# Performance work log

Hardware: AMD Instinct MI355X
Metric: run time of the kernel (lower is better)

The kernel has to match this reference:

```python
import jax, jax.numpy as jnp
import numpy as np

LN_EPS = 1e-5
NEG_INF = -1e30


def setup_inputs() -> dict:
    key = jax.random.key(0)
    k_adj, k_feat, k_mask, k_w = jax.random.split(key, 4)
    B, N, H, R, L = 8, 400, 768, 46, 2
    adj = jax.random.uniform(k_adj, (B, N, N, R), dtype=jnp.float32)
    feature = jax.random.normal(k_feat, (B, N, H), dtype=jnp.float32)
    dmask = (jax.random.uniform(k_mask, (B, 1, N)) > 0.1).astype(jnp.float32)
    # per-layer, per-relation Linear(H, H, bias=False) weights, applied as x @ W
    W = jax.random.normal(k_w, (L, R, H, H), dtype=jnp.float32) / np.sqrt(H)
    return {"adj": adj, "feature": feature, "dmask": dmask, "W": W}


def reference(adj, feature, dmask, W):
    # adj: [B,N,N,R] -> [B,R,N,N]; dmask: [B,1,N] masks key/column axis
    B, N, _, R = adj.shape
    a = jnp.transpose(adj, (0, 3, 1, 2))           # [B,R,N,N]
    m = dmask[:, None, :, :]                        # [B,1,1,N]
    logits = a * m + (1.0 - m) * NEG_INF
    att = jax.nn.softmax(logits, axis=-1)           # [B,R,N,N] (layer-invariant)

    x = feature
    num_layers = W.shape[0]
    for layer in range(num_layers):
        # grouped per-relation linear: h[b,r,n,k] = feature[b,n,h] @ W[layer,r,h,k]
        h = jnp.einsum('bnh,rhk->brnk', x, W[layer])
        h = jax.nn.relu(jnp.einsum('brnm,brmk->brnk', att, h))
        addition = h.sum(axis=1)                    # sum over relations -> [B,N,H]
        z = jax.nn.relu(addition) / R
        # LayerNorm without affine params
        mu = jnp.mean(z, axis=-1, keepdims=True)
        var = jnp.var(z, axis=-1, keepdims=True)
        x = (z - mu) / jnp.sqrt(var + LN_EPS)
        # dropout is identity in eval mode
    return x
```

## Files before the change

kernel.cpp:

```cpp
#include <hip/hip_runtime.h>
#include <stdint.h>

#define BS 8
#define NN 400
#define HH 768
#define RR 46
#define MPAD 416
#define MFLAT2 3328
#define LDW2 3328
#define PADM 402

typedef _Float16 half8 __attribute__((ext_vector_type(8)));
typedef _Float16 half4v __attribute__((ext_vector_type(4)));
typedef float floatx4 __attribute__((ext_vector_type(4)));

__device__ __forceinline__ void async16(const void* g, void* l) {
  __builtin_amdgcn_global_load_lds((const __attribute__((address_space(1))) uint32_t*)g,
                                   (__attribute__((address_space(3))) uint32_t*)l, 16, 0, 0);
}

__device__ __forceinline__ int xcd_work(int flat, int nwg) {
  int q = nwg >> 3, rem = nwg & 7;
  int xcd = flat & 7, slot = flat >> 3;
  return (xcd < rem ? xcd * (q + 1) : rem * (q + 1) + (xcd - rem) * q) + slot;
}

__device__ __forceinline__ void vm_wait(int ahead) {
  if (ahead >= 2) asm volatile("s_waitcnt vmcnt(8)" ::: "memory");
  else if (ahead == 1) asm volatile("s_waitcnt vmcnt(4)" ::: "memory");
  else asm volatile("s_waitcnt vmcnt(0)" ::: "memory");
}
__device__ __forceinline__ void vm_wait2(int ahead) {
  if (ahead >= 2) asm volatile("s_waitcnt vmcnt(4)" ::: "memory");
  else if (ahead == 1) asm volatile("s_waitcnt vmcnt(2)" ::: "memory");
  else asm volatile("s_waitcnt vmcnt(0)" ::: "memory");
}
#define BAR_TOP() { __builtin_amdgcn_s_barrier(); __builtin_amdgcn_sched_barrier(0); }
#define BAR_BOT() { asm volatile("s_waitcnt lgkmcnt(0)" ::: "memory"); \
                    __builtin_amdgcn_s_barrier(); __builtin_amdgcn_sched_barrier(0); }
#define BAR_ONE() { asm volatile("s_barrier" ::: "memory"); __builtin_amdgcn_sched_barrier(0); }

__device__ __forceinline__ void stage_tile(const _Float16* __restrict__ g, int ld, int rowbase,
                                           int maxrow, int kbase, _Float16* lds, int t) {
  int w = t >> 6, lane = t & 63;
#pragma unroll
  for (int j = 0; j < 2; ++j) {
    int chunk = w * 2 + j;
    int eo = chunk * 512 + lane * 8;
    int row = eo >> 5;
    int col = eo & 31;
    int grow = rowbase + row;
    grow = grow > maxrow ? maxrow : grow;
    async16(g + (size_t)grow * ld + kbase + col, lds + chunk * 512);
  }
}

__device__ __forceinline__ void mma_tiles(const _Float16* As, const _Float16* Bs, int lane,
                                          int wr, int wc, floatx4 acc[4][4]) {
  int arow = wr + (lane & 15);
  int brow = wc + (lane & 15);
  int kcol = (lane >> 4) * 8;
  half8 a[4], b[4];
#pragma unroll
  for (int i = 0; i < 4; ++i) a[i] = *(const half8*)&As[(arow + i * 16) * 32 + kcol];
#pragma unroll
  for (int i = 0; i < 4; ++i) b[i] = *(const half8*)&Bs[(brow + i * 16) * 32 + kcol];
#pragma unroll
  for (int i = 0; i < 4; ++i)
#pragma unroll
    for (int j = 0; j < 4; ++j)
      acc[i][j] = __builtin_amdgcn_mfma_f32_16x16x32_f16(a[i], b[j], acc[i][j], 0, 0, 0);
}

__device__ __forceinline__ void mma8(const _Float16* As, const _Float16* Bs, int lane,
                                     int wr, int wc, floatx4 acc[4][2]) {
  int arow = wr + (lane & 15);
  int brow = wc + (lane & 15);
  int kcol = (lane >> 4) * 8;
  half8 a[4], b[2];
#pragma unroll
  for (int i = 0; i < 4; ++i) a[i] = *(const half8*)&As[(arow + i * 16) * 32 + kcol];
#pragma unroll
  for (int j = 0; j < 2; ++j) b[j] = *(const half8*)&Bs[(brow + j * 16) * 32 + kcol];
#pragma unroll
  for (int i = 0; i < 4; ++i)
#pragma unroll
    for (int j = 0; j < 2; ++j)
      acc[i][j] = __builtin_amdgcn_mfma_f32_16x16x32_f16(a[i], b[j], acc[i][j], 0, 0, 0);
}

__global__ __launch_bounds__(256) void conv_w(const float* __restrict__ W, _Float16* __restrict__ Wt) {
  __shared__ float tl[32][33];
  int t = threadIdx.x;
  int lr = blockIdx.y;
  int tr = blockIdx.x / 24, tc = blockIdx.x % 24;
  const float* src = W + (size_t)lr * HH * HH;
  _Float16* dst = Wt + (size_t)lr * HH * HH;
  int rl = t >> 5, cl = t & 31;
#pragma unroll
  for (int j = 0; j < 4; ++j)
    tl[rl + 8 * j][cl] = src[(size_t)(tr * 32 + rl + 8 * j) * HH + tc * 32 + cl];
  __syncthreads();
#pragma unroll
  for (int j = 0; j < 4; ++j)
    dst[(size_t)(tc * 32 + rl + 8 * j) * HH + tr * 32 + cl] = (_Float16)tl[cl][rl + 8 * j];
}

__global__ void conv_x(const float* __restrict__ f, _Float16* __restrict__ x16) {
  int i4 = blockIdx.x * 256 + threadIdx.x;
  int row = i4 / 192;
  int c4 = i4 - row * 192;
  int b = row / 416;
  int m = row - b * 416;
  half4v h = {};
  if (m < NN) {
    float4 v = *(const float4*)(f + ((size_t)(b * NN + m) * HH) + c4 * 4);
    h[0] = (_Float16)v.x; h[1] = (_Float16)v.y; h[2] = (_Float16)v.z; h[3] = (_Float16)v.w;
  }
  *(half4v*)&x16[(size_t)row * HH + c4 * 4] = h;
}

__global__ __launch_bounds__(512) void att_softmax(const float* __restrict__ adj,
                                                   const float* __restrict__ dmask,
                                                   _Float16* __restrict__ att) {
  __shared__ _Float16 sE[RR * PADM];
  __shared__ float sM[NN];
  int t = threadIdx.x;
  int n = blockIdx.x, b = blockIdx.y;
  const float* arow = adj + ((size_t)b * NN + n) * NN * RR;
  for (int i = t; i < NN; i += 512) sM[i] = dmask[b * NN + i];
  __syncthreads();
  for (int e0 = t * 4; e0 < NN * RR; e0 += 2048) {
    float4 v = *(const float4*)(arow + e0);
    float vv[4] = {v.x, v.y, v.z, v.w};
#pragma unroll
    for (int j = 0; j < 4; ++j) {
      int e = e0 + j;
      int m = e / RR;
      int r = e - m * RR;
      float val = sM[m] > 0.5f ? __expf(vv[j]) : 0.0f;
      sE[r * PADM + m] = (_Float16)val;
    }
  }
  __syncthreads();
  int lane = t & 63, wid = t >> 6;
  for (int r = wid; r < RR; r += 8) {
    const _Float16* row = &sE[r * PADM];
    float s = 0.f;
    for (int m = lane; m < NN; m += 64) s += (float)row[m];
#pragma unroll
    for (int o = 32; o; o >>= 1) s += __shfl_xor(s, o);
    float inv = 1.0f / s;
    _Float16* orow = att + (((size_t)b * RR + r) * NN + n) * MPAD;
    for (int m2 = lane * 2; m2 < MPAD; m2 += 128) {
      _Float16 lo = (_Float16)0.f, hi = (_Float16)0.f;
      if (m2 < NN) lo = (_Float16)((float)row[m2] * inv);
      if (m2 + 1 < NN) hi = (_Float16)((float)row[m2 + 1] * inv);
      union { _Float16 h[2]; uint32_t u; } pk;
      pk.h[0] = lo; pk.h[1] = hi;
      *(uint32_t*)&orow[m2] = pk.u;
    }
  }
}

__global__ __launch_bounds__(256) void gemm_xw(const _Float16* __restrict__ x16,
                                               const _Float16* __restrict__ Wt,
                                               _Float16* __restrict__ h1T, int layer, int r0, int rbase) {
  __shared__ __align__(16) char smraw[49152];
  int t = threadIdx.x;
  int work = xcd_work(blockIdx.x, gridDim.x);
  int r_i = work / 156;
  int rem = work - r_i * 156;
  int r = r0 + r_i;
  int mtile = rem / 6, ntile = rem % 6;
  const _Float16* A = x16;
  const _Float16* Bp = Wt + ((size_t)layer * RR + r) * HH * HH;
  int lane = t & 63, w = t >> 6;
  int wr = (w >> 1) * 64, wc = (w & 1) * 64;
  floatx4 acc[4][4] = {};
  stage_tile(A, HH, mtile * 128, MFLAT2 - 1, 0, (_Float16*)smraw, t);
  stage_tile(Bp, HH, ntile * 128, HH - 1, 0, (_Float16*)(smraw + 8192), t);
  stage_tile(A, HH, mtile * 128, MFLAT2 - 1, 32, (_Float16*)(smraw + 16384), t);
  stage_tile(Bp, HH, ntile * 128, HH - 1, 32, (_Float16*)(smraw + 24576), t);
  int cur = 0, stb = 2;
  for (int ks = 0; ks < 24; ++ks) {
    if (ks + 2 < 24) {
      char* nb = smraw + stb * 16384;
      stage_tile(A, HH, mtile * 128, MFLAT2 - 1, (ks + 2) * 32, (_Float16*)nb, t);
      stage_tile(Bp, HH, ntile * 128, HH - 1, (ks + 2) * 32, (_Float16*)(nb + 8192), t);
      stb = stb == 2 ? 0 : stb + 1;
    }
    vm_wait(ks + 2 < 24 ? 2 : (ks + 1 < 24 ? 1 : 0));
    BAR_TOP();
    char* cb = smraw + cur * 16384;
    mma_tiles((const _Float16*)cb, (const _Float16*)(cb + 8192), lane, wr, wc, acc);
    BAR_BOT();
    cur = cur == 2 ? 0 : cur + 1;
  }
  _Float16* outl = (_Float16*)smraw;
#pragma unroll
  for (int i = 0; i < 4; ++i) {
#pragma unroll
    for (int j = 0; j < 4; ++j) {
      int rl = wr + i * 16 + (lane >> 4) * 4;
      int cl = wc + j * 16 + (lane & 15);
      half4v v = {(_Float16)acc[i][j][0], (_Float16)acc[i][j][1],
                  (_Float16)acc[i][j][2], (_Float16)acc[i][j][3]};
      *(half4v*)&outl[cl * 136 + rl] = v;
    }
  }
  __syncthreads();
  _Float16* outp = h1T + (size_t)(r - rbase) * HH * LDW2;
#pragma unroll
  for (int pass = 0; pass < 8; ++pass) {
    int c = pass * 16 + (t >> 4);
    int ml = (t & 15) * 8;
    int gm = mtile * 128 + ml;
    int gn = ntile * 128 + c;
    half8 v = *(const half8*)&outl[c * 136 + ml];
    *(half8*)&outp[(size_t)gn * LDW2 + gm] = v;
  }
}

__global__ __launch_bounds__(512, 4) void gemm_att(const _Float16* __restrict__ att,
                                                   const _Float16* __restrict__ h1T,
                                                   float* __restrict__ partials, size_t psz,
                                                   int rs, int rcount, int rbase, int accflag,
                                                   int ngroups) {
  __shared__ __align__(16) char smraw[65536];
  int t = threadIdx.x;
  int work = xcd_work(blockIdx.x, gridDim.x);
  int ntile = work % 6;
  int tmp = work / 6;
  int mtile = tmp & 3; tmp >>= 2;
  int g = tmp % ngroups;
  int b = tmp / ngroups;
  int rbeg = rs + (g * rcount) / ngroups;
  int rend = rs + ((g + 1) * rcount) / ngroups;
  int nr = rend - rbeg;
  int total = nr * 13;
  float* part = partials + (size_t)g * psz;
  int lane = t & 63, w = t >> 6;
  int wr = (w >> 2) * 64, wc = (w & 3) * 32;
  floatx4 acc[4][2] = {}, sum[4][2] = {};

  int srow = w * 16 + (lane >> 2), scol = (lane & 3) * 8;
  int ga = mtile * 128 + srow; ga = ga > NN - 1 ? NN - 1 : ga;
  int gb = ntile * 128 + srow;
  const _Float16* pa = att + ((size_t)b * RR + rbeg) * NN * MPAD + (size_t)ga * MPAD + scol;
  const _Float16* pb = h1T + (size_t)(rbeg - rbase) * HH * LDW2 + (size_t)gb * LDW2 + b * MPAD + scol;
  int nsk = 0;
  auto issue = [&](int buf) {
    char* lb = smraw + (buf << 14) + w * 1024;
    async16(pa, lb);
    async16(pb, lb + 8192);
    if (++nsk == 13) { nsk = 0; pa += (size_t)NN * MPAD - 384; pb += (size_t)HH * LDW2 - 384; }
    else { pa += 32; pb += 32; }
  };

  issue(0); issue(1); issue(2);
  vm_wait2(2);
  BAR_ONE();
  int cks = 0;
  for (int s = 0; s < total; ++s) {
    if (s + 3 < total) issue((s + 3) & 3);
    char* cb = smraw + ((s & 3) << 14);
    __builtin_amdgcn_s_setprio(1);
    mma8((const _Float16*)cb, (const _Float16*)(cb + 8192), lane, wr, wc, acc);
    __builtin_amdgcn_s_setprio(0);
    if (cks == 12) {
#pragma unroll
      for (int i = 0; i < 4; ++i)
#pragma unroll
        for (int j = 0; j < 2; ++j) {
#pragma unroll
          for (int q2 = 0; q2 < 4; ++q2) sum[i][j][q2] += fmaxf(acc[i][j][q2], 0.0f);
          acc[i][j] = (floatx4){0.f, 0.f, 0.f, 0.f};
        }
      cks = 0;
    } else ++cks;
    if (s + 1 < total) {
      int ahead = total - s - 2;
      vm_wait2(ahead > 2 ? 2 : ahead);
      BAR_ONE();
    }
  }
#pragma unroll
  for (int i = 0; i < 4; ++i) {
    int rl = wr + i * 16 + (lane >> 4) * 4;
    int grow = mtile * 128 + rl;
#pragma unroll
    for (int j = 0; j < 2; ++j) {
      int gcol = ntile * 128 + wc + j * 16 + (lane & 15);
#pragma unroll
      for (int q2 = 0; q2 < 4; ++q2) {
        if (grow + q2 < NN) {
          size_t idx = ((size_t)b * NN + grow + q2) * HH + gcol;
          float v = sum[i][j][q2];
          if (accflag) v += part[idx];
          part[idx] = v;
        }
      }
    }
  }
}

__global__ __launch_bounds__(256) void lnorm(const float* __restrict__ partials, size_t psz, int np,
                                             _Float16* __restrict__ x16, float* __restrict__ out) {
  int row = blockIdx.x;
  int t = threadIdx.x;
  int b = row / NN;
  int xrow = row + b * 16;
  float v[3];
  float s = 0.f, s2 = 0.f;
#pragma unroll
  for (int j = 0; j < 3; ++j) {
    float a = 0.f;
    for (int gidx = 0; gidx < np; ++gidx) a += partials[(size_t)gidx * psz + (size_t)row * HH + t + j * 256];
    v[j] = fmaxf(a, 0.f) * (1.0f / RR);
    s += v[j];
    s2 += v[j] * v[j];
  }
#pragma unroll
  for (int o = 32; o; o >>= 1) {
    s += __shfl_xor(s, o);
    s2 += __shfl_xor(s2, o);
  }
  __shared__ float rs_[4], rs2_[4];
  int lane = t & 63, wid = t >> 6;
  if (!lane) { rs_[wid] = s; rs2_[wid] = s2; }
  __syncthreads();
  s = rs_[0] + rs_[1] + rs_[2] + rs_[3];
  s2 = rs2_[0] + rs2_[1] + rs2_[2] + rs2_[3];
  float mu = s * (1.0f / HH);
  float var = s2 * (1.0f / HH) - mu * mu;
  float rstd = rsqrtf(var + 1e-5f);
#pragma unroll
  for (int j = 0; j < 3; ++j) {
    float o = (v[j] - mu) * rstd;
    out[(size_t)row * HH + t + j * 256] = o;
    x16[(size_t)xrow * HH + t + j * 256] = (_Float16)o;
  }
}

extern "C" void kernel_launch(void* const* d_in, const int* in_sizes, int n_in,
                              void* d_out, int out_size, void* d_ws, size_t ws_size,
                              hipStream_t stream) {
  const float* adj = (const float*)d_in[0];
  const float* feature = (const float*)d_in[1];
  const float* dmask = (const float*)d_in[2];
  const float* W = (const float*)d_in[3];
  float* out = (float*)d_out;

  uintptr_t base = (uintptr_t)d_ws;
  uintptr_t p = base;
  auto alloc = [&](size_t bytes) -> void* {
    uintptr_t q = (p + 255) & ~(uintptr_t)255;
    p = q + bytes;
    return (void*)q;
  };
  _Float16* att = (_Float16*)alloc((size_t)BS * RR * NN * MPAD * 2);
  _Float16* Wt = (_Float16*)alloc((size_t)2 * RR * HH * HH * 2);
  _Float16* x16 = (_Float16*)alloc((size_t)MFLAT2 * HH * 2);
  size_t psz = (size_t)(BS * NN) * HH;
  size_t pszB = psz * 4;
  size_t used = p - base;
  size_t rem = ws_size > used ? ws_size - used : 0;
  size_t perR = (size_t)HH * LDW2 * 2;
  size_t h1full = (size_t)RR * perR;

  conv_w<<<dim3(576, 2 * RR), 256, 0, stream>>>(W, Wt);
  conv_x<<<MFLAT2 * HH / 4 / 256, 256, 0, stream>>>(feature, x16);
  att_softmax<<<dim3(NN, BS), 512, 0, stream>>>(adj, dmask, att);

  if (rem >= h1full + 4 * pszB + 512) {
    _Float16* h1T = (_Float16*)alloc(h1full);
    int ngroups = (int)(((ws_size - (p - base)) - 256) / pszB);
    if (ngroups > 8) ngroups = 8;
    float* partials = (float*)alloc((size_t)ngroups * pszB);
    for (int layer = 0; layer < 2; ++layer) {
      gemm_xw<<<156 * RR, 256, 0, stream>>>(x16, Wt, h1T, layer, 0, 0);
      gemm_att<<<6 * 4 * ngroups * BS, 512, 0, stream>>>(att, h1T, partials, psz, 0, RR, 0, 0, ngroups);
      lnorm<<<BS * NN, 256, 0, stream>>>(partials, psz, ngroups, x16, out);
    }
  } else {
    float* partials = (float*)alloc(pszB);
    size_t rem2 = ws_size > (p - base) ? ws_size - (p - base) : 0;
    int RCmax = (int)(rem2 / perR);
    if (RCmax > RR) RCmax = RR;
    if (RCmax < 1) RCmax = 1;
    _Float16* h1T = (_Float16*)alloc((size_t)RCmax * perR);
    for (int layer = 0; layer < 2; ++layer) {
      for (int r0 = 0; r0 < RR; r0 += RCmax) {
        int rc = RR - r0 < RCmax ? RR - r0 : RCmax;
        gemm_xw<<<156 * rc, 256, 0, stream>>>(x16, Wt, h1T, layer, r0, r0);
        gemm_att<<<6 * 4 * 1 * BS, 512, 0, stream>>>(att, h1T, partials, psz, r0, rc, r0, r0 > 0, 1);
      }
      lnorm<<<BS * NN, 256, 0, stream>>>(partials, psz, 1, x16, out);
    }
  }
}
```

Before: 1.052 ms.

## Swizzle LDS tile layout to avoid bank conflicts and batch adj loads in softmax

The staged 32-wide fp16 tiles in LDS now use an XOR swizzle on the 8-element column chunk. The global source addresses are permuted to match, so the LDS slot order stays fixed, and the MFMA operand reads apply the same XOR. This is meant to remove LDS bank conflicts on the half8 fragment reads. Separately, the attention softmax kernel issues all nine float4 loads of the adj row up front, before the barrier, to raise memory-level parallelism. The cost is more registers in that kernel.

```diff
diff --git a/kernel.cpp b/kernel.cpp
--- a/kernel.cpp
+++ b/kernel.cpp
@@ -40,18 +40,18 @@
                     __builtin_amdgcn_s_barrier(); __builtin_amdgcn_sched_barrier(0); }
 #define BAR_ONE() { asm volatile("s_barrier" ::: "memory"); __builtin_amdgcn_sched_barrier(0); }
 
+
 __device__ __forceinline__ void stage_tile(const _Float16* __restrict__ g, int ld, int rowbase,
                                            int maxrow, int kbase, _Float16* lds, int t) {
   int w = t >> 6, lane = t & 63;
+  int swz = ((lane & 3) ^ ((lane >> 3) & 3)) * 8;
 #pragma unroll
   for (int j = 0; j < 2; ++j) {
     int chunk = w * 2 + j;
-    int eo = chunk * 512 + lane * 8;
-    int row = eo >> 5;
-    int col = eo & 31;
+    int row = chunk * 16 + (lane >> 2);
     int grow = rowbase + row;
     grow = grow > maxrow ? maxrow : grow;
-    async16(g + (size_t)grow * ld + kbase + col, lds + chunk * 512);
+    async16(g + (size_t)grow * ld + kbase + swz, lds + chunk * 512);
   }
 }
 
@@ -59,12 +59,12 @@
                                           int wr, int wc, floatx4 acc[4][4]) {
   int arow = wr + (lane & 15);
   int brow = wc + (lane & 15);
-  int kcol = (lane >> 4) * 8;
+  int kswz = ((lane >> 4) ^ ((lane >> 1) & 3)) * 8;
   half8 a[4], b[4];
 #pragma unroll
-  for (int i = 0; i < 4; ++i) a[i] = *(const half8*)&As[(arow + i * 16) * 32 + kcol];
-#pragma unroll
-  for (int i = 0; i < 4; ++i) b[i] = *(const half8*)&Bs[(brow + i * 16) * 32 + kcol];
+  for (int i = 0; i < 4; ++i) a[i] = *(const half8*)&As[(arow + i * 16) * 32 + kswz];
+#pragma unroll
+  for (int i = 0; i < 4; ++i) b[i] = *(const half8*)&Bs[(brow + i * 16) * 32 + kswz];
 #pragma unroll
   for (int i = 0; i < 4; ++i)
 #pragma unroll
@@ -76,12 +76,12 @@
                                      int wr, int wc, floatx4 acc[4][2]) {
   int arow = wr + (lane & 15);
   int brow = wc + (lane & 15);
-  int kcol = (lane >> 4) * 8;
+  int kswz = ((lane >> 4) ^ ((lane >> 1) & 3)) * 8;
   half8 a[4], b[2];
 #pragma unroll
-  for (int i = 0; i < 4; ++i) a[i] = *(const half8*)&As[(arow + i * 16) * 32 + kcol];
-#pragma unroll
-  for (int j = 0; j < 2; ++j) b[j] = *(const half8*)&Bs[(brow + j * 16) * 32 + kcol];
+  for (int i = 0; i < 4; ++i) a[i] = *(const half8*)&As[(arow + i * 16) * 32 + kswz];
+#pragma unroll
+  for (int j = 0; j < 2; ++j) b[j] = *(const half8*)&Bs[(brow + j * 16) * 32 + kswz];
 #pragma unroll
   for (int i = 0; i < 4; ++i)
 #pragma unroll
@@ -127,19 +127,29 @@
   __shared__ float sM[NN];
   int t = threadIdx.x;
   int n = blockIdx.x, b = blockIdx.y;
-  const float* arow = adj + ((size_t)b * NN + n) * NN * RR;
+  const float4* src = (const float4*)(adj + ((size_t)b * NN + n) * NN * RR);
   for (int i = t; i < NN; i += 512) sM[i] = dmask[b * NN + i];
+  float4 v[9];
+#pragma unroll
+  for (int k = 0; k < 9; ++k) {
+    int idx = t + k * 512;
+    if (idx < NN * RR / 4) v[k] = src[idx];
+  }
   __syncthreads();
-  for (int e0 = t * 4; e0 < NN * RR; e0 += 2048) {
-    float4 v = *(const float4*)(arow + e0);
-    float vv[4] = {v.x, v.y, v.z, v.w};
-#pragma unroll
-    for (int j = 0; j < 4; ++j) {
-      int e = e0 + j;
-      int m = e / RR;
-      int r = e - m * RR;
-      float val = sM[m] > 0.5f ? __expf(vv[j]) : 0.0f;
-      sE[r * PADM + m] = (_Float16)val;
+#pragma unroll
+  for (int k = 0; k < 9; ++k) {
+    int idx = t + k * 512;
+    if (idx < NN * RR / 4) {
+      int e0 = idx * 4;
+      float vv[4] = {v[k].x, v[k].y, v[k].z, v[k].w};
+#pragma unroll
+      for (int j = 0; j < 4; ++j) {
+        int e = e0 + j;
+        int m = e / RR;
+        int r = e - m * RR;
+        float val = sM[m] > 0.5f ? __expf(vv[j]) : 0.0f;
+        sE[r * PADM + m] = (_Float16)val;
+      }
     }
   }
   __syncthreads();
@@ -244,7 +254,8 @@
   int wr = (w >> 2) * 64, wc = (w & 3) * 32;
   floatx4 acc[4][2] = {}, sum[4][2] = {};
 
-  int srow = w * 16 + (lane >> 2), scol = (lane & 3) * 8;
+  int srow = w * 16 + (lane >> 2);
+  int scol = ((lane & 3) ^ ((lane >> 3) & 3)) * 8;
   int ga = mtile * 128 + srow; ga = ga > NN - 1 ? NN - 1 : ga;
   int gb = ntile * 128 + srow;
   const _Float16* pa = att + ((size_t)b * RR + rbeg) * NN * MPAD + (size_t)ga * MPAD + scol;
```

After: 1.041 ms. No clear change (-1.0%).
